# Kernel tuning notes

Hardware: AMD Instinct MI355X
Metric: run time of the kernel (lower is better)

The kernel has to match this reference:

```python
import jax, jax.numpy as jnp
import numpy as np

ALPHA = 0.2  # leaky relu slope
NEG_BIG = -9e15


def setup_inputs() -> dict:
    key = jax.random.key(0)
    k1, k2, k3, k4 = jax.random.split(key, 4)
    B, N, Fin, Fout = 8, 2048, 128, 128
    h = jax.random.normal(k1, (B, N, Fin), dtype=jnp.float32)
    adj = jax.random.randint(k2, (N, N), 0, 2, dtype=jnp.int32)
    # xavier_uniform with gain=1.414
    limW = 1.414 * np.sqrt(6.0 / (Fin + Fout))
    W = jax.random.uniform(k3, (Fin, Fout), minval=-limW, maxval=limW, dtype=jnp.float32)
    lima = 1.414 * np.sqrt(6.0 / (2 * Fout + 1))
    a = jax.random.uniform(k4, (2 * Fout, 1), minval=-lima, maxval=lima, dtype=jnp.float32)
    return {"h": h, "adj": adj, "W": W, "a": a}


def reference(h, adj, W, a):
    # Wh: [B, N, F]
    Wh = jnp.einsum("bnf,fo->bno", h, W)
    Fout = W.shape[1]
    a1, a2 = a[:Fout, 0], a[Fout:, 0]  # [F], [F]
    # Additive score decomposition (same math as concat trick):
    # e[b,i,j] = leakyrelu(Wh_i . a1 + Wh_j . a2)
    s1 = Wh @ a1  # [B, N] (source/query part)
    s2 = Wh @ a2  # [B, N] (target part)
    e = s1[:, :, None] + s2[:, None, :]  # [B, N, N]
    e = jnp.where(e > 0, e, ALPHA * e)   # leaky relu
    e = jnp.where(adj[None, :, :] > 0, e, NEG_BIG)
    attention = jax.nn.softmax(e, axis=2)  # [B, N, N]
    # dropout is identity in eval mode
    h_prime = jnp.einsum("bij,bjf->bif", attention, Wh)
    return h_prime
```

## Files before the change

### kernel.cpp

```cpp
#include <hip/hip_runtime.h>
#include <hip/hip_bf16.h>
#include <stdint.h>

#define ALPHA 0.2f

typedef __attribute__((ext_vector_type(8))) short bf16x8;
typedef __attribute__((ext_vector_type(4))) float f32x4;

__device__ __forceinline__ short f2bf(float f) {
    union { float f; uint32_t u; } c; c.f = f;
    uint32_t u = c.u + 0x7FFF + ((c.u >> 16) & 1);
    return (short)(u >> 16);
}

__device__ __forceinline__ uint32_t pk_bf16(float lo, float hi) {
    union { float f; uint32_t u; } a, b;
    a.f = lo; b.f = hi;
    return __builtin_amdgcn_perm(b.u + 0x8000u, a.u + 0x8000u, 0x07060302u);
}

__global__ __launch_bounds__(256) void pack_adj_kernel(
        const int* __restrict__ adj, uint8_t* __restrict__ bytes,
        const float* __restrict__ W, short* __restrict__ WTg) {
    int t = blockIdx.x * 256 + threadIdx.x;
    const int4* a4 = reinterpret_cast<const int4*>(adj) + (size_t)t * 2;
    int4 x0 = a4[0], x1 = a4[1];
    uint32_t m = 0;
    m |= (x0.x > 0) ? 1u   : 0u;  m |= (x0.y > 0) ? 2u   : 0u;
    m |= (x0.z > 0) ? 4u   : 0u;  m |= (x0.w > 0) ? 8u   : 0u;
    m |= (x1.x > 0) ? 16u  : 0u;  m |= (x1.y > 0) ? 32u  : 0u;
    m |= (x1.z > 0) ? 64u  : 0u;  m |= (x1.w > 0) ? 128u : 0u;
    bytes[t] = (uint8_t)m;

    if (blockIdx.x < 64) {
        int idx = blockIdx.x * 256 + threadIdx.x;
        int k = idx >> 7, f = idx & 127;
        WTg[f * 128 + k] = f2bf(W[k * 128 + f]);
    }
}

__global__ __launch_bounds__(256) void wh_kernel(
        const float* __restrict__ h, const short* __restrict__ WTg,
        const float* __restrict__ a, short* __restrict__ whT,
        float* __restrict__ s1g, float* __restrict__ s2g) {
    __shared__ float sred[4][2][16];
    __shared__ short tr[4][32][24];

    int tid = threadIdx.x, wid = tid >> 6, lane = tid & 63;
    int q = lane >> 4, n = lane & 15;
    int bb = blockIdx.x & 7;
    int tile = blockIdx.x >> 3;
    int rb = bb * 2048 + tile * 16;
    int row = rb + n;

    f32x4 acc[2] = {};
    #pragma unroll
    for (int kc = 0; kc < 4; ++kc) {
        const float* hp = h + (size_t)row * 128 + kc * 32 + q * 8;
        float4 h0 = reinterpret_cast<const float4*>(hp)[0];
        float4 h1 = reinterpret_cast<const float4*>(hp)[1];
        bf16x8 afrag;
        afrag[0] = f2bf(h0.x); afrag[1] = f2bf(h0.y);
        afrag[2] = f2bf(h0.z); afrag[3] = f2bf(h0.w);
        afrag[4] = f2bf(h1.x); afrag[5] = f2bf(h1.y);
        afrag[6] = f2bf(h1.z); afrag[7] = f2bf(h1.w);
        #pragma unroll
        for (int u = 0; u < 2; ++u) {
            int t = wid * 2 + u;
            bf16x8 bfrag = *reinterpret_cast<const bf16x8*>(
                WTg + (t * 16 + n) * 128 + kc * 32 + q * 8);
            acc[u] = __builtin_amdgcn_mfma_f32_16x16x32_bf16(afrag, bfrag, acc[u], 0, 0, 0);
        }
    }

    float p1[4] = {0.f, 0.f, 0.f, 0.f}, p2[4] = {0.f, 0.f, 0.f, 0.f};
    #pragma unroll
    for (int u = 0; u < 2; ++u) {
        int c = (wid * 2 + u) * 16 + n;
        float a1c = a[c] * 1.442695041f;
        float a2c = a[128 + c] * 1.442695041f;
        #pragma unroll
        for (int r = 0; r < 4; ++r) {
            p1[r] += acc[u][r] * a1c;
            p2[r] += acc[u][r] * a2c;
        }
    }
    #pragma unroll
    for (int d = 1; d < 16; d <<= 1) {
        #pragma unroll
        for (int r = 0; r < 4; ++r) {
            p1[r] += __shfl_xor(p1[r], d);
            p2[r] += __shfl_xor(p2[r], d);
        }
    }
    if (n == 0) {
        #pragma unroll
        for (int r = 0; r < 4; ++r) {
            sred[wid][0][q * 4 + r] = p1[r];
            sred[wid][1][q * 4 + r] = p2[r];
        }
    }

    #pragma unroll
    for (int u = 0; u < 2; ++u)
        #pragma unroll
        for (int r = 0; r < 4; ++r)
            tr[wid][u * 16 + n][q * 4 + r] = f2bf(acc[u][r]);
    __syncthreads();

    if (wid == 0 && lane < 16) {
        float v1 = 0.f, v2 = 0.f;
        #pragma unroll
        for (int v = 0; v < 4; ++v) { v1 += sred[v][0][lane]; v2 += sred[v][1][lane]; }
        s1g[rb + lane] = v1;
        s2g[rb + lane] = v2;
    }

    int jr = rb & 2047;
    int fl = lane & 31, jh = lane >> 5;
    bf16x8 v = *reinterpret_cast<const bf16x8*>(&tr[wid][fl][jh * 8]);
    int f = wid * 32 + fl;
    int t = f >> 4, nn = f & 15;
    int jc = jr >> 5;
    int qg = ((jr & 31) >> 3) + jh;
    *reinterpret_cast<bf16x8*>(
        whT + (size_t)(bb * 64 + jc) * 4096 + t * 512 + qg * 128 + nn * 8) = v;
}

__device__ __forceinline__ void load_nb(const char* gb, int chunk, int lane,
                                        bf16x8* nb) {
    const char* cb = gb + (size_t)chunk * 8192 + lane * 16;
    #pragma unroll
    for (int t = 0; t < 8; ++t)
        nb[t] = *reinterpret_cast<const bf16x8*>(cb + t * 1024);
}

__global__ __launch_bounds__(256, 2) void attn_kernel(
        const short* __restrict__ whT, const float* __restrict__ s1g,
        const float* __restrict__ s2g, const uint8_t* __restrict__ adjb,
        float* __restrict__ out) {
    __shared__ uint32_t mlds[32 * 65];
    __shared__ float s2lds[2048];
    __shared__ float dslds[4][16];
    __shared__ f32x4 cbuf[1024];

    int tid = threadIdx.x, wid = tid >> 6, lane = tid & 63;
    int q = lane >> 4, n = lane & 15;
    int rg = wid & 1, jh = wid >> 1;
    int b  = blockIdx.x & 7;
    int ib = (blockIdx.x >> 3) * 32;
    int row = ib + rg * 16 + n;

    float s1A = s1g[b * 2048 + row];
    const char* gbase = reinterpret_cast<const char*>(whT) + (size_t)b * 524288;

    {
        int r = tid >> 3, sub = tid & 7;
        const uint4* src = reinterpret_cast<const uint4*>(
            adjb + (size_t)(ib + r) * 256 + sub * 32);
        uint4 v0 = src[0], v1 = src[1];
        uint32_t* dst = &mlds[r * 65 + sub * 8];
        dst[0] = v0.x; dst[1] = v0.y; dst[2] = v0.z; dst[3] = v0.w;
        dst[4] = v1.x; dst[5] = v1.y; dst[6] = v1.z; dst[7] = v1.w;
    }
    {
        const float* s2b = s2g + b * 2048;
        float4 v0 = *reinterpret_cast<const float4*>(s2b + tid * 8);
        float4 v1 = *reinterpret_cast<const float4*>(s2b + tid * 8 + 4);
        *reinterpret_cast<float4*>(&s2lds[tid * 8])     = v0;
        *reinterpret_cast<float4*>(&s2lds[tid * 8 + 4]) = v1;
    }
    __syncthreads();

    f32x4 acc[8] = {};
    float ds = 0.f;
    int mrow = (rg * 16 + n) * 65 + jh * 32;
    int cb0 = jh * 32;

    bf16x8 nbA[8], nbB[8];
    load_nb(gbase, cb0, lane, nbA);

    #pragma unroll 1
    for (int cc = 0; cc < 32; cc += 2) {
        load_nb(gbase, cb0 + cc + 1, lane, nbB);

        {
            int c = cc;
            uint32_t mA = mlds[mrow + c] >> (q * 8);
            int sb = (cb0 + c) * 32 + q * 8;
            float4 s2a = *reinterpret_cast<const float4*>(&s2lds[sb]);
            float4 s2c = *reinterpret_cast<const float4*>(&s2lds[sb + 4]);
            float s2arr[8] = {s2a.x, s2a.y, s2a.z, s2a.w,
                              s2c.x, s2c.y, s2c.z, s2c.w};
            float p[8];
            #pragma unroll
            for (int j = 0; j < 8; ++j) {
                float e = s1A + s2arr[j];
                e = fmaxf(e, ALPHA * e);
                float v = ((mA >> j) & 1) ? __builtin_amdgcn_exp2f(e) : 0.0f;
                ds += v; p[j] = v;
            }
            union { uint32_t u32[4]; bf16x8 v; } cv;
            #pragma unroll
            for (int pp = 0; pp < 4; ++pp)
                cv.u32[pp] = pk_bf16(p[2 * pp], p[2 * pp + 1]);
            #pragma unroll
            for (int t = 0; t < 8; ++t)
                acc[t] = __builtin_amdgcn_mfma_f32_16x16x32_bf16(cv.v, nbA[t], acc[t], 0, 0, 0);
        }

        if (cc + 2 < 32) load_nb(gbase, cb0 + cc + 2, lane, nbA);

        {
            int c = cc + 1;
            uint32_t mA = mlds[mrow + c] >> (q * 8);
            int sb = (cb0 + c) * 32 + q * 8;
            float4 s2a = *reinterpret_cast<const float4*>(&s2lds[sb]);
            float4 s2c = *reinterpret_cast<const float4*>(&s2lds[sb + 4]);
            float s2arr[8] = {s2a.x, s2a.y, s2a.z, s2a.w,
                              s2c.x, s2c.y, s2c.z, s2c.w};
            float p[8];
            #pragma unroll
            for (int j = 0; j < 8; ++j) {
                float e = s1A + s2arr[j];
                e = fmaxf(e, ALPHA * e);
                float v = ((mA >> j) & 1) ? __builtin_amdgcn_exp2f(e) : 0.0f;
                ds += v; p[j] = v;
            }
            union { uint32_t u32[4]; bf16x8 v; } cv;
            #pragma unroll
            for (int pp = 0; pp < 4; ++pp)
                cv.u32[pp] = pk_bf16(p[2 * pp], p[2 * pp + 1]);
            #pragma unroll
            for (int t = 0; t < 8; ++t)
                acc[t] = __builtin_amdgcn_mfma_f32_16x16x32_bf16(cv.v, nbB[t], acc[t], 0, 0, 0);
        }
    }

    ds += __shfl_xor(ds, 16); ds += __shfl_xor(ds, 32);
    if (q == 0) dslds[wid][n] = ds;

    __syncthreads();
    if (jh == 1) {
        #pragma unroll
        for (int i = 0; i < 8; ++i)
            cbuf[(rg * 8 + i) * 64 + lane] = acc[i];
    }
    __syncthreads();
    if (jh == 0) {
        #pragma unroll
        for (int i = 0; i < 8; ++i)
            acc[i] += cbuf[(rg * 8 + i) * 64 + lane];

        float dtot = dslds[rg][n] + dslds[2 + rg][n];
        float rd[4];
        #pragma unroll
        for (int r = 0; r < 4; ++r)
            rd[r] = 1.0f / __shfl(dtot, q * 4 + r);

        size_t ob = ((size_t)b * 2048 + ib + rg * 16) * 128;
        #pragma unroll
        for (int t = 0; t < 8; ++t)
            #pragma unroll
            for (int r = 0; r < 4; ++r)
                out[ob + (size_t)(q * 4 + r) * 128 + t * 16 + n] = acc[t][r] * rd[r];
    }
}

extern "C" void kernel_launch(void* const* d_in, const int* in_sizes, int n_in,
                              void* d_out, int out_size, void* d_ws, size_t ws_size,
                              hipStream_t stream) {
    const float* h   = (const float*)d_in[0];
    const int*   adj = (const int*)d_in[1];
    const float* W   = (const float*)d_in[2];
    const float* a   = (const float*)d_in[3];
    float* out = (float*)d_out;

    char* ws = (char*)d_ws;
    short* whT = (short*)ws;
    float* s1  = (float*)(ws + 4194304);
    float* s2  = (float*)(ws + 4259840);
    uint8_t* bytes = (uint8_t*)(ws + 4325376);
    short* WTg = (short*)(ws + 4849664);

    pack_adj_kernel<<<2048, 256, 0, stream>>>(adj, bytes, W, WTg);
    wh_kernel<<<1024, 256, 0, stream>>>(h, WTg, a, whT, s1, s2);
    attn_kernel<<<512, 256, 0, stream>>>(whT, s1, s2, bytes, out);
}
```

Before: 105.6 us.

## Split columns across four waves, each covering both row groups to reuse B fragments

Each wave now processes both 16-row groups over a quarter of the column chunks, instead of one row group over half the chunks. Every loaded Wh fragment then feeds two MFMAs, halving global/L2 loads of Wh per block. In exchange, accumulator registers double (16 f32x4), which may push register pressure against the 2-blocks-per-SM launch bound. The cross-wave reduction also grows to three partials through a larger LDS buffer, while one barrier is removed.

```diff
diff --git a/kernel.cpp b/kernel.cpp
--- a/kernel.cpp
+++ b/kernel.cpp
@@ -141,17 +141,16 @@
         float* __restrict__ out) {
     __shared__ uint32_t mlds[32 * 65];
     __shared__ float s2lds[2048];
-    __shared__ float dslds[4][16];
-    __shared__ f32x4 cbuf[1024];
+    __shared__ float dslds[4][2][16];
+    __shared__ f32x4 cbuf[3][16][64];
 
     int tid = threadIdx.x, wid = tid >> 6, lane = tid & 63;
     int q = lane >> 4, n = lane & 15;
-    int rg = wid & 1, jh = wid >> 1;
     int b  = blockIdx.x & 7;
     int ib = (blockIdx.x >> 3) * 32;
-    int row = ib + rg * 16 + n;
-
-    float s1A = s1g[b * 2048 + row];
+
+    float s1A0 = s1g[b * 2048 + ib + n];
+    float s1A1 = s1g[b * 2048 + ib + 16 + n];
     const char* gbase = reinterpret_cast<const char*>(whT) + (size_t)b * 524288;
 
     {
@@ -172,98 +171,98 @@
     }
     __syncthreads();
 
-    f32x4 acc[8] = {};
-    float ds = 0.f;
-    int mrow = (rg * 16 + n) * 65 + jh * 32;
-    int cb0 = jh * 32;
+    f32x4 acc0[8] = {}, acc1[8] = {};
+    float ds0 = 0.f, ds1 = 0.f;
+    int gc0 = wid * 16;
+    int mrow0 = n * 65, mrow1 = (16 + n) * 65;
 
     bf16x8 nbA[8], nbB[8];
-    load_nb(gbase, cb0, lane, nbA);
+    load_nb(gbase, gc0, lane, nbA);
+
+#define PROCESS(C, NB)                                                        \
+    {                                                                         \
+        int gc = gc0 + (C);                                                   \
+        uint32_t mA0 = mlds[mrow0 + gc] >> (q * 8);                           \
+        uint32_t mA1 = mlds[mrow1 + gc] >> (q * 8);                           \
+        int sb = gc * 32 + q * 8;                                             \
+        float4 s2a = *reinterpret_cast<const float4*>(&s2lds[sb]);            \
+        float4 s2c = *reinterpret_cast<const float4*>(&s2lds[sb + 4]);        \
+        float s2arr[8] = {s2a.x, s2a.y, s2a.z, s2a.w,                         \
+                          s2c.x, s2c.y, s2c.z, s2c.w};                        \
+        float p0[8], p1[8];                                                   \
+        _Pragma("unroll")                                                     \
+        for (int j = 0; j < 8; ++j) {                                         \
+            float e0 = s1A0 + s2arr[j];                                       \
+            e0 = fmaxf(e0, ALPHA * e0);                                       \
+            float v0 = ((mA0 >> j) & 1) ? __builtin_amdgcn_exp2f(e0) : 0.0f;  \
+            ds0 += v0; p0[j] = v0;                                            \
+            float e1 = s1A1 + s2arr[j];                                       \
+            e1 = fmaxf(e1, ALPHA * e1);                                       \
+            float v1 = ((mA1 >> j) & 1) ? __builtin_amdgcn_exp2f(e1) : 0.0f;  \
+            ds1 += v1; p1[j] = v1;                                            \
+        }                                                                     \
+        union { uint32_t u32[4]; bf16x8 v; } cv0, cv1;                        \
+        _Pragma("unroll")                                                     \
+        for (int pp = 0; pp < 4; ++pp) {                                      \
+            cv0.u32[pp] = pk_bf16(p0[2 * pp], p0[2 * pp + 1]);                \
+            cv1.u32[pp] = pk_bf16(p1[2 * pp], p1[2 * pp + 1]);                \
+        }                                                                     \
+        _Pragma("unroll")                                                     \
+        for (int t = 0; t < 8; ++t) {                                         \
+            acc0[t] = __builtin_amdgcn_mfma_f32_16x16x32_bf16(                \
+                cv0.v, (NB)[t], acc0[t], 0, 0, 0);                            \
+            acc1[t] = __builtin_amdgcn_mfma_f32_16x16x32_bf16(                \
+                cv1.v, (NB)[t], acc1[t], 0, 0, 0);                            \
+        }                                                                     \
+    }
 
     #pragma unroll 1
-    for (int cc = 0; cc < 32; cc += 2) {
-        load_nb(gbase, cb0 + cc + 1, lane, nbB);
-
-        {
-            int c = cc;
-            uint32_t mA = mlds[mrow + c] >> (q * 8);
-            int sb = (cb0 + c) * 32 + q * 8;
-            float4 s2a = *reinterpret_cast<const float4*>(&s2lds[sb]);
-            float4 s2c = *reinterpret_cast<const float4*>(&s2lds[sb + 4]);
-            float s2arr[8] = {s2a.x, s2a.y, s2a.z, s2a.w,
-                              s2c.x, s2c.y, s2c.z, s2c.w};
-            float p[8];
+    for (int cc = 0; cc < 16; cc += 2) {
+        load_nb(gbase, gc0 + cc + 1, lane, nbB);
+        PROCESS(cc, nbA)
+        if (cc + 2 < 16) load_nb(gbase, gc0 + cc + 2, lane, nbA);
+        PROCESS(cc + 1, nbB)
+    }
+#undef PROCESS
+
+    ds0 += __shfl_xor(ds0, 16); ds0 += __shfl_xor(ds0, 32);
+    ds1 += __shfl_xor(ds1, 16); ds1 += __shfl_xor(ds1, 32);
+    if (q == 0) { dslds[wid][0][n] = ds0; dslds[wid][1][n] = ds1; }
+
+    if (wid != 0) {
+        #pragma unroll
+        for (int t = 0; t < 8; ++t) {
+            cbuf[wid - 1][t][lane]     = acc0[t];
+            cbuf[wid - 1][8 + t][lane] = acc1[t];
+        }
+    }
+    __syncthreads();
+    if (wid == 0) {
+        #pragma unroll
+        for (int w = 0; w < 3; ++w)
             #pragma unroll
-            for (int j = 0; j < 8; ++j) {
-                float e = s1A + s2arr[j];
-                e = fmaxf(e, ALPHA * e);
-                float v = ((mA >> j) & 1) ? __builtin_amdgcn_exp2f(e) : 0.0f;
-                ds += v; p[j] = v;
+            for (int t = 0; t < 8; ++t) {
+                acc0[t] += cbuf[w][t][lane];
+                acc1[t] += cbuf[w][8 + t][lane];
             }
-            union { uint32_t u32[4]; bf16x8 v; } cv;
-            #pragma unroll
-            for (int pp = 0; pp < 4; ++pp)
-                cv.u32[pp] = pk_bf16(p[2 * pp], p[2 * pp + 1]);
-            #pragma unroll
-            for (int t = 0; t < 8; ++t)
-                acc[t] = __builtin_amdgcn_mfma_f32_16x16x32_bf16(cv.v, nbA[t], acc[t], 0, 0, 0);
-        }
-
-        if (cc + 2 < 32) load_nb(gbase, cb0 + cc + 2, lane, nbA);
-
-        {
-            int c = cc + 1;
-            uint32_t mA = mlds[mrow + c] >> (q * 8);
-            int sb = (cb0 + c) * 32 + q * 8;
-            float4 s2a = *reinterpret_cast<const float4*>(&s2lds[sb]);
-            float4 s2c = *reinterpret_cast<const float4*>(&s2lds[sb + 4]);
-            float s2arr[8] = {s2a.x, s2a.y, s2a.z, s2a.w,
-                              s2c.x, s2c.y, s2c.z, s2c.w};
-            float p[8];
-            #pragma unroll
-            for (int j = 0; j < 8; ++j) {
-                float e = s1A + s2arr[j];
-                e = fmaxf(e, ALPHA * e);
-                float v = ((mA >> j) & 1) ? __builtin_amdgcn_exp2f(e) : 0.0f;
-                ds += v; p[j] = v;
-            }
-            union { uint32_t u32[4]; bf16x8 v; } cv;
-            #pragma unroll
-            for (int pp = 0; pp < 4; ++pp)
-                cv.u32[pp] = pk_bf16(p[2 * pp], p[2 * pp + 1]);
-            #pragma unroll
-            for (int t = 0; t < 8; ++t)
-                acc[t] = __builtin_amdgcn_mfma_f32_16x16x32_bf16(cv.v, nbB[t], acc[t], 0, 0, 0);
-        }
-    }
-
-    ds += __shfl_xor(ds, 16); ds += __shfl_xor(ds, 32);
-    if (q == 0) dslds[wid][n] = ds;
-
-    __syncthreads();
-    if (jh == 1) {
-        #pragma unroll
-        for (int i = 0; i < 8; ++i)
-            cbuf[(rg * 8 + i) * 64 + lane] = acc[i];
-    }
-    __syncthreads();
-    if (jh == 0) {
-        #pragma unroll
-        for (int i = 0; i < 8; ++i)
-            acc[i] += cbuf[(rg * 8 + i) * 64 + lane];
-
-        float dtot = dslds[rg][n] + dslds[2 + rg][n];
-        float rd[4];
-        #pragma unroll
-        for (int r = 0; r < 4; ++r)
-            rd[r] = 1.0f / __shfl(dtot, q * 4 + r);
-
-        size_t ob = ((size_t)b * 2048 + ib + rg * 16) * 128;
+
+        float dtot0 = dslds[0][0][n] + dslds[1][0][n] + dslds[2][0][n] + dslds[3][0][n];
+        float dtot1 = dslds[0][1][n] + dslds[1][1][n] + dslds[2][1][n] + dslds[3][1][n];
+        float rd0[4], rd1[4];
+        #pragma unroll
+        for (int r = 0; r < 4; ++r) {
+            rd0[r] = 1.0f / __shfl(dtot0, q * 4 + r);
+            rd1[r] = 1.0f / __shfl(dtot1, q * 4 + r);
+        }
+
+        size_t ob = ((size_t)b * 2048 + ib) * 128;
         #pragma unroll
         for (int t = 0; t < 8; ++t)
             #pragma unroll
-            for (int r = 0; r < 4; ++r)
-                out[ob + (size_t)(q * 4 + r) * 128 + t * 16 + n] = acc[t][r] * rd[r];
+            for (int r = 0; r < 4; ++r) {
+                out[ob + (size_t)(q * 4 + r) * 128 + t * 16 + n]        = acc0[t][r] * rd0[r];
+                out[ob + (size_t)(16 + q * 4 + r) * 128 + t * 16 + n]   = acc1[t][r] * rd1[r];
+            }
     }
 }
 
```

Result: no change. 104.3 us (-1.2%).
